# Performance work log

Measured on AMD Instinct MI355X. Metric: run time of the kernel, lower is better.

Reference implementation:

```python
import jax, jax.numpy as jnp
import numpy as np

DIM = 2048
N_HEADS = 32
N_KV_HEADS = 8
HEAD_DIM = DIM // N_HEADS  # 64
GROUP = N_HEADS // N_KV_HEADS  # 4
ROPE_BASE = 10000.0


def setup_inputs() -> dict:
    key = jax.random.key(0)
    k1, k2, k3, k4, k5 = jax.random.split(key, 5)
    b, s = 1, 2048
    scale = 1.0 / np.sqrt(DIM)
    return {
        "x": jax.random.normal(k1, (b, s, DIM), dtype=jnp.float32),
        # weights stored as (in, out); equivalent math to torch Linear (x @ W.T)
        "wq": jax.random.normal(k2, (DIM, N_HEADS * HEAD_DIM), dtype=jnp.float32) * scale,
        "wk": jax.random.normal(k3, (DIM, N_KV_HEADS * HEAD_DIM), dtype=jnp.float32) * scale,
        "wv": jax.random.normal(k4, (DIM, N_KV_HEADS * HEAD_DIM), dtype=jnp.float32) * scale,
        "wo": jax.random.normal(k5, (N_HEADS * HEAD_DIM, DIM), dtype=jnp.float32) * scale,
    }


def _rope_cos_sin(seq_len, dtype):
    inv_freq = 1.0 / (ROPE_BASE ** (jnp.arange(0, HEAD_DIM, 2, dtype=jnp.float32) / HEAD_DIM))
    t = jnp.arange(seq_len, dtype=jnp.float32)
    freqs = jnp.outer(t, inv_freq)              # [s, hd/2]
    emb = jnp.concatenate([freqs, freqs], -1)   # [s, hd]
    return jnp.cos(emb).astype(dtype), jnp.sin(emb).astype(dtype)


def _rotate_half(x):
    x1, x2 = x[..., : HEAD_DIM // 2], x[..., HEAD_DIM // 2 :]
    return jnp.concatenate([-x2, x1], axis=-1)


def reference(x, wq, wk, wv, wo):
    b, s, _ = x.shape
    q = (x @ wq).reshape(b, s, N_HEADS, HEAD_DIM)
    k = (x @ wk).reshape(b, s, N_KV_HEADS, HEAD_DIM)
    v = (x @ wv).reshape(b, s, N_KV_HEADS, HEAD_DIM)

    cos, sin = _rope_cos_sin(s, x.dtype)
    cos = cos[None, :, None, :]  # [1, s, 1, hd] broadcast over batch & heads
    sin = sin[None, :, None, :]
    q = q * cos + _rotate_half(q) * sin
    k = k * cos + _rotate_half(k) * sin

    # GQA: repeat KV heads (repeat_interleave along head dim)
    k = jnp.repeat(k, GROUP, axis=2)  # [b, s, n_heads, hd]
    v = jnp.repeat(v, GROUP, axis=2)

    q = q.transpose(0, 2, 1, 3)  # [b, h, s, d]
    k = k.transpose(0, 2, 1, 3)
    v = v.transpose(0, 2, 1, 3)

    scores = jnp.einsum("bhqd,bhkd->bhqk", q, k) / jnp.sqrt(jnp.asarray(HEAD_DIM, x.dtype))
    attn = jax.nn.softmax(scores, axis=-1)
    out = jnp.einsum("bhqk,bhkd->bhqd", attn, v)
    out = out.transpose(0, 2, 1, 3).reshape(b, s, N_HEADS * HEAD_DIM)
    return out @ wo
```

## Files before the change

kernel.cpp:

```cpp
#include <hip/hip_runtime.h>
#include <hip/hip_bf16.h>

typedef __bf16 bf16x8 __attribute__((ext_vector_type(8)));
typedef __bf16 bf16x4 __attribute__((ext_vector_type(4)));
typedef __bf16 bf16x2 __attribute__((ext_vector_type(2)));
typedef float fx4 __attribute__((ext_vector_type(4)));
typedef float fx16 __attribute__((ext_vector_type(16)));

#define AS1 __attribute__((address_space(1)))
#define AS3 __attribute__((address_space(3)))

__global__ __launch_bounds__(256) void prep(const float4* __restrict__ X, __bf16* __restrict__ Xb,
                                            const float* __restrict__ wq, const float* __restrict__ wk,
                                            const float* __restrict__ wv, const float* __restrict__ wo,
                                            __bf16* __restrict__ WqkvT, __bf16* __restrict__ WoT) {
    const int bx = blockIdx.x;
    if (bx < 4096) {
        const int i = bx * 256 + threadIdx.x;
        const float4 v = X[i];
        bf16x4 o = { (__bf16)v.x, (__bf16)v.y, (__bf16)v.z, (__bf16)v.w };
        *(bf16x4*)(Xb + (size_t)i * 4) = o;
        return;
    }
    constexpr int K = 2048;
    __shared__ float t[64][33];
    const int tt = bx - 4096;
    const float* W; __bf16* Wt; int N, loc;
    if (tt < 2048)      { W = wq; Wt = WqkvT;                       N = 2048; loc = tt; }
    else if (tt < 2560) { W = wk; Wt = WqkvT + (size_t)2048 * 2048; N = 512;  loc = tt - 2048; }
    else if (tt < 3072) { W = wv; Wt = WqkvT + (size_t)2560 * 2048; N = 512;  loc = tt - 2560; }
    else                { W = wo; Wt = WoT;                         N = 2048; loc = tt - 3072; }
    const int k0 = (loc & 31) * 64, n0 = (loc >> 5) * 32;
    const int tx = threadIdx.x & 31, ty = threadIdx.x >> 5;
#pragma unroll
    for (int i = 0; i < 8; ++i)
        t[ty + i * 8][tx] = W[(size_t)(k0 + ty + i * 8) * N + n0 + tx];
    __syncthreads();
#pragma unroll
    for (int i = 0; i < 4; ++i) {
        const int nn = ty + i * 8;
        bf16x2 o = { (__bf16)t[tx * 2][nn], (__bf16)t[tx * 2 + 1][nn] };
        *(bf16x2*)&Wt[(size_t)(n0 + nn) * K + k0 + tx * 2] = o;
    }
}

#define GEMM_SETUP(Aptr, Btptr)                                                              \
    constexpr int K = 2048;                                                                  \
    __shared__ __align__(16) __bf16 sm[4][8192];                                  \
    const int tid = threadIdx.x;                                                             \
    const int wave = tid >> 6, lane = tid & 63;                                              \
    const int quad = lane >> 4, l16 = lane & 15;                                             \
    const int wm = (wave >> 1) * 64, wn = (wave & 1) * 64;                                   \
    fx4 acc[4][4] = {};                                                                      \
    const int r4 = lane >> 2;                                                                \
    const int c8s = ((lane & 3) ^ ((r4 >> 1) & 3)) * 8;                                      \
    const __bf16* csrc[4]; int cdst[4];                                                      \
    _Pragma("unroll")                                                                        \
    for (int it = 0; it < 4; ++it) {                                                         \
        const int idx = wave * 4 + it;                                                       \
        if (idx < 8) { csrc[it] = (Aptr) + (size_t)(m0 + idx * 16 + r4) * K + c8s;           \
                       cdst[it] = idx * 512 + lane * 8; }                                    \
        else         { csrc[it] = (Btptr) + (size_t)(n0 + (idx - 8) * 16 + r4) * K + c8s;    \
                       cdst[it] = 4096 + (idx - 8) * 512 + lane * 8; }                       \
    }                                                                                        \
    const int colr = (quad ^ ((l16 >> 1) & 3)) * 8;                                          \
    const int arow = (wm + l16) * 32 + colr;                                                 \
    const int brow = 4096 + (wn + l16) * 32 + colr;                                          \
    auto compute = [&](const __bf16* cb) {                                                   \
        bf16x8 af[4], bfr[4];                                                                \
        _Pragma("unroll") for (int i = 0; i < 4; ++i) af[i]  = *(const bf16x8*)&cb[arow + i * 512]; \
        _Pragma("unroll") for (int j = 0; j < 4; ++j) bfr[j] = *(const bf16x8*)&cb[brow + j * 512]; \
        __builtin_amdgcn_s_setprio(1);                                                       \
        _Pragma("unroll") for (int i = 0; i < 4; ++i)                                        \
            _Pragma("unroll") for (int j = 0; j < 4; ++j)                                    \
                acc[i][j] = __builtin_amdgcn_mfma_f32_16x16x32_bf16(af[i], bfr[j], acc[i][j], 0, 0, 0); \
        __builtin_amdgcn_s_setprio(0);                                                       \
    };                                                                                       \
    _Pragma("unroll")                                                                        \
    for (int pt = 0; pt < 3; ++pt)                                                           \
        _Pragma("unroll")                                                                    \
        for (int it = 0; it < 4; ++it)                                                       \
            __builtin_amdgcn_global_load_lds((const AS1 void*)(csrc[it] + pt * 32),          \
                                             (AS3 void*)&sm[pt][cdst[it]], 16, 0, 0);        \
    _Pragma("unroll 1")                                                                      \
    for (int tq = 0; tq < 15; ++tq) {                                                        \
        const int t0 = tq * 4;                                                               \
        _Pragma("unroll")                                                                    \
        for (int u = 0; u < 4; ++u) {                                                        \
            asm volatile("s_waitcnt vmcnt(8) lgkmcnt(0)" ::: "memory");                      \
            __builtin_amdgcn_s_barrier();                                                    \
            __builtin_amdgcn_sched_barrier(0);                                               \
            const int tile = t0 + u + 3;                                                     \
            const int kofs = tile * 32;                                                      \
            _Pragma("unroll")                                                                \
            for (int it = 0; it < 4; ++it)                                                   \
                __builtin_amdgcn_global_load_lds((const AS1 void*)(csrc[it] + kofs),         \
                                                 (AS3 void*)&sm[(u + 3) & 3][cdst[it]], 16, 0, 0); \
            compute(sm[u]);                                                                  \
        }                                                                                    \
    }                                                                                        \
    {                            \
        asm volatile("s_waitcnt vmcnt(8) lgkmcnt(0)" ::: "memory");                          \
        __builtin_amdgcn_s_barrier();                                                        \
        __builtin_amdgcn_sched_barrier(0);                                                   \
        _Pragma("unroll")                                                                    \
        for (int it = 0; it < 4; ++it)                                                       \
            __builtin_amdgcn_global_load_lds((const AS1 void*)(csrc[it] + 63 * 32),          \
                                             (AS3 void*)&sm[3][cdst[it]], 16, 0, 0);         \
        compute(sm[0]);                                                                      \
    }                                                                                        \
    asm volatile("s_waitcnt vmcnt(8) lgkmcnt(0)" ::: "memory"); __builtin_amdgcn_s_barrier();\
    __builtin_amdgcn_sched_barrier(0); compute(sm[1]);                                       \
    asm volatile("s_waitcnt vmcnt(4) lgkmcnt(0)" ::: "memory"); __builtin_amdgcn_s_barrier();\
    __builtin_amdgcn_sched_barrier(0); compute(sm[2]);                                       \
    asm volatile("s_waitcnt vmcnt(0) lgkmcnt(0)" ::: "memory"); __builtin_amdgcn_s_barrier();\
    __builtin_amdgcn_sched_barrier(0); compute(sm[3]);

__global__ __launch_bounds__(256, 2) void gemm_qkv(const __bf16* __restrict__ A, const __bf16* __restrict__ Bt,
                                                   __bf16* __restrict__ Qr, __bf16* __restrict__ Kr,
                                                   __bf16* __restrict__ Vt) {
    const int bid = blockIdx.x;
    const int swz = (bid & 7) * 48 + (bid >> 3);
    const int m0 = (swz & 15) * 128, n0 = (swz >> 4) * 128;

    GEMM_SETUP(A, Bt)

    const int col64 = n0 + wn;
    if (col64 < 2560) {
        const bool isQ = col64 < 2048;
        const float scale = isQ ? 0.18033688011112042f : 1.0f;
        __bf16* base = isQ ? (Qr + (size_t)(col64 >> 6) * 2048 * 64)
                           : (Kr + (size_t)((col64 - 2048) >> 6) * 2048 * 64);
#pragma unroll
        for (int jj = 0; jj < 2; ++jj) {
            const int dlo = jj * 16 + l16;
            const float inv = __builtin_amdgcn_exp2f(-(float)dlo * 0.41524101186092029f);
#pragma unroll
            for (int i = 0; i < 4; ++i)
#pragma unroll
                for (int r = 0; r < 4; ++r) {
                    const int s = m0 + wm + i * 16 + quad * 4 + r;
                    float sn, cs;
                    __sincosf((float)s * inv, &sn, &cs);
                    const float lo = acc[i][jj][r], hv = acc[i][jj + 2][r];
                    base[(size_t)s * 64 + dlo]      = (__bf16)((lo * cs - hv * sn) * scale);
                    base[(size_t)s * 64 + dlo + 32] = (__bf16)((hv * cs + lo * sn) * scale);
                }
        }
    } else {
        __bf16* vb = Vt + (size_t)((col64 - 2560) >> 6) * 64 * 2048;
#pragma unroll
        for (int i = 0; i < 4; ++i)
#pragma unroll
            for (int j = 0; j < 4; ++j) {
                const int d = j * 16 + l16;
                const int s0 = m0 + wm + i * 16 + quad * 4;
                bf16x4 p;
#pragma unroll
                for (int r = 0; r < 4; ++r) p[r] = (__bf16)acc[i][j][r];
                *(bf16x4*)&vb[(size_t)d * 2048 + s0] = p;
            }
    }
}

__global__ __launch_bounds__(256, 2) void gemm_out(const __bf16* __restrict__ A, const __bf16* __restrict__ Bt,
                                                   float* __restrict__ C) {
    const int bid = blockIdx.x;
    const int swz = (bid & 7) * 32 + (bid >> 3);
    const int m0 = (swz & 15) * 128, n0 = (swz >> 4) * 128;

    GEMM_SETUP(A, Bt)

#pragma unroll
    for (int i = 0; i < 4; ++i)
#pragma unroll
        for (int j = 0; j < 4; ++j) {
            const int row = m0 + wm + i * 16 + quad * 4;
            const int col = n0 + wn + j * 16 + l16;
#pragma unroll
            for (int r = 0; r < 4; ++r)
                C[(size_t)(row + r) * 2048 + col] = acc[i][j][r];
        }
}

__global__ __launch_bounds__(512, 4) void flash_attn(const __bf16* __restrict__ Qr, const __bf16* __restrict__ Kr,
                                                     const __bf16* __restrict__ Vt, __bf16* __restrict__ O) {
    constexpr int S = 2048;
    __shared__ __align__(16) __bf16 smem[2][4 * 64 * 72];
    const int qt = blockIdx.x, h = blockIdx.y, kvh = h >> 2;
    const int tid = threadIdx.x, wave = tid >> 6, lane = tid & 63;
    const int grp = wave >> 2, w4 = wave & 3;
    const int l32 = lane & 31, hi = lane >> 5;
    const int goff = grp * 2 * 4608;

    const int qrow = qt * 128 + w4 * 32 + l32;
    const __bf16* qptr = Qr + ((size_t)h * S + qrow) * 64;
    bf16x8 qf[4];
#pragma unroll
    for (int kc = 0; kc < 4; ++kc) qf[kc] = *(const bf16x8*)(qptr + kc * 16 + hi * 8);

    const __bf16* Kbase = Kr + (size_t)kvh * S * 64;
    const __bf16* Vbase = Vt + (size_t)kvh * 64 * S;

    const int gtid = tid & 255;
    const int krow = gtid >> 3;
    const int kcol = (gtid & 7) * 8;
    const int vslot = (kcol & 48) | ((kcol & 8) >> 1);

    bf16x8 kreg0 = *(const bf16x8*)(Kbase + (size_t)(grp * 64 + krow) * 64 + kcol);
    bf16x8 kreg1 = *(const bf16x8*)(Kbase + (size_t)(grp * 64 + 32 + krow) * 64 + kcol);
    bf16x8 vreg0 = *(const bf16x8*)(Vbase + (size_t)krow * S + grp * 64 + kcol);
    bf16x8 vreg1 = *(const bf16x8*)(Vbase + (size_t)(32 + krow) * S + grp * 64 + kcol);

    fx16 ov0, ov1;
#pragma unroll
    for (int i = 0; i < 16; ++i) { ov0[i] = 0.f; ov1[i] = 0.f; }
    float l_acc = 0.f;

    {
        __bf16* nK = &smem[0][goff];
        __bf16* nV = nK + 4608;
        *(bf16x8*)&nK[krow * 72 + kcol] = kreg0;
        *(bf16x8*)&nK[(32 + krow) * 72 + kcol] = kreg1;
        bf16x4 v0lo = { vreg0[0], vreg0[1], vreg0[2], vreg0[3] };
        bf16x4 v0hi = { vreg0[4], vreg0[5], vreg0[6], vreg0[7] };
        bf16x4 v1lo = { vreg1[0], vreg1[1], vreg1[2], vreg1[3] };
        bf16x4 v1hi = { vreg1[4], vreg1[5], vreg1[6], vreg1[7] };
        *(bf16x4*)&nV[krow * 72 + vslot]            = v0lo;
        *(bf16x4*)&nV[krow * 72 + vslot + 8]        = v0hi;
        *(bf16x4*)&nV[(32 + krow) * 72 + vslot]     = v1lo;
        *(bf16x4*)&nV[(32 + krow) * 72 + vslot + 8] = v1hi;
        const int kt1 = 2 + grp;
        kreg0 = *(const bf16x8*)(Kbase + (size_t)(kt1 * 64 + krow) * 64 + kcol);
        kreg1 = *(const bf16x8*)(Kbase + (size_t)(kt1 * 64 + 32 + krow) * 64 + kcol);
        vreg0 = *(const bf16x8*)(Vbase + (size_t)krow * S + kt1 * 64 + kcol);
        vreg1 = *(const bf16x8*)(Vbase + (size_t)(32 + krow) * S + kt1 * 64 + kcol);
    }
    asm volatile("s_waitcnt lgkmcnt(0)" ::: "memory");
    __builtin_amdgcn_s_barrier();
    __builtin_amdgcn_sched_barrier(0);

    for (int it = 0; it < 16; ++it) {
        __bf16* lKg = &smem[it & 1][goff];
        __bf16* lVg = lKg + 4608;

        if (it + 1 < 16) {
            __bf16* nK = &smem[(it + 1) & 1][goff];
            __bf16* nV = nK + 4608;
            *(bf16x8*)&nK[krow * 72 + kcol] = kreg0;
            *(bf16x8*)&nK[(32 + krow) * 72 + kcol] = kreg1;
            bf16x4 v0lo = { vreg0[0], vreg0[1], vreg0[2], vreg0[3] };
            bf16x4 v0hi = { vreg0[4], vreg0[5], vreg0[6], vreg0[7] };
            bf16x4 v1lo = { vreg1[0], vreg1[1], vreg1[2], vreg1[3] };
            bf16x4 v1hi = { vreg1[4], vreg1[5], vreg1[6], vreg1[7] };
            *(bf16x4*)&nV[krow * 72 + vslot]            = v0lo;
            *(bf16x4*)&nV[krow * 72 + vslot + 8]        = v0hi;
            *(bf16x4*)&nV[(32 + krow) * 72 + vslot]     = v1lo;
            *(bf16x4*)&nV[(32 + krow) * 72 + vslot + 8] = v1hi;
            const int it2 = (it + 2 < 16) ? it + 2 : 15;
            const int ktn = it2 * 2 + grp;
            kreg0 = *(const bf16x8*)(Kbase + (size_t)(ktn * 64 + krow) * 64 + kcol);
            kreg1 = *(const bf16x8*)(Kbase + (size_t)(ktn * 64 + 32 + krow) * 64 + kcol);
            vreg0 = *(const bf16x8*)(Vbase + (size_t)krow * S + ktn * 64 + kcol);
            vreg1 = *(const bf16x8*)(Vbase + (size_t)(32 + krow) * S + ktn * 64 + kcol);
        }

        fx16 sc0, sc1;
#pragma unroll
        for (int i = 0; i < 16; ++i) { sc0[i] = 0.f; sc1[i] = 0.f; }
        __builtin_amdgcn_s_setprio(1);
#pragma unroll
        for (int kc = 0; kc < 4; ++kc) {
            const bf16x8 a0 = *(const bf16x8*)&lKg[l32 * 72 + kc * 16 + hi * 8];
            const bf16x8 a1 = *(const bf16x8*)&lKg[(32 + l32) * 72 + kc * 16 + hi * 8];
            sc0 = __builtin_amdgcn_mfma_f32_32x32x16_bf16(a0, qf[kc], sc0, 0, 0, 0);
            sc1 = __builtin_amdgcn_mfma_f32_32x32x16_bf16(a1, qf[kc], sc1, 0, 0, 0);
        }
        __builtin_amdgcn_s_setprio(0);

#pragma unroll
        for (int h2 = 0; h2 < 2; ++h2) {
#pragma unroll
            for (int c = 0; c < 2; ++c) {
                bf16x8 pb;
#pragma unroll
                for (int j = 0; j < 8; ++j) {
                    const float sv = h2 ? sc1[c * 8 + j] : sc0[c * 8 + j];
                    const float p = __builtin_amdgcn_exp2f(sv);
                    l_acc += p;
                    pb[j] = (__bf16)p;
                }
                const int kcv = h2 * 2 + c;
                const bf16x8 va0 = *(const bf16x8*)&lVg[l32 * 72 + kcv * 16 + hi * 8];
                const bf16x8 va1 = *(const bf16x8*)&lVg[(32 + l32) * 72 + kcv * 16 + hi * 8];
                __builtin_amdgcn_s_setprio(1);
                ov0 = __builtin_amdgcn_mfma_f32_32x32x16_bf16(va0, pb, ov0, 0, 0, 0);
                ov1 = __builtin_amdgcn_mfma_f32_32x32x16_bf16(va1, pb, ov1, 0, 0, 0);
                __builtin_amdgcn_s_setprio(0);
            }
        }
        asm volatile("s_waitcnt lgkmcnt(0)" ::: "memory");
        __builtin_amdgcn_s_barrier();
        __builtin_amdgcn_sched_barrier(0);
    }

    const float l_pair = l_acc + __shfl_xor(l_acc, 32, 64);

    fx4* lO = (fx4*)&smem[0][0];
    float* lL = (float*)(&smem[0][0] + 16384);
    if (grp == 1) {
#pragma unroll
        for (int ic = 0; ic < 4; ++ic) {
            fx4 c0, c1;
#pragma unroll
            for (int r = 0; r < 4; ++r) { c0[r] = ov0[ic * 4 + r]; c1[r] = ov1[ic * 4 + r]; }
            lO[(ic * 4 + w4) * 64 + lane] = c0;
            lO[((ic + 4) * 4 + w4) * 64 + lane] = c1;
        }
        if (hi == 0) lL[w4 * 32 + l32] = l_pair;
    }
    __syncthreads();
    if (grp == 0) {
#pragma unroll
        for (int ic = 0; ic < 4; ++ic) {
            const fx4 c0 = lO[(ic * 4 + w4) * 64 + lane];
            const fx4 c1 = lO[((ic + 4) * 4 + w4) * 64 + lane];
#pragma unroll
            for (int r = 0; r < 4; ++r) { ov0[ic * 4 + r] += c0[r]; ov1[ic * 4 + r] += c1[r]; }
        }
        const float inv_l = 1.0f / (l_pair + lL[w4 * 32 + l32]);
#pragma unroll
        for (int dt = 0; dt < 2; ++dt)
#pragma unroll
            for (int rg2 = 0; rg2 < 4; ++rg2) {
                bf16x4 o4;
#pragma unroll
                for (int r = 0; r < 4; ++r)
                    o4[r] = (__bf16)((dt ? ov1[rg2 * 4 + r] : ov0[rg2 * 4 + r]) * inv_l);
                const int col = h * 64 + dt * 32 + rg2 * 8 + hi * 4;
                *(bf16x4*)(O + (size_t)qrow * 2048 + col) = o4;
            }
    }
}

extern "C" void kernel_launch(void* const* d_in, const int* in_sizes, int n_in,
                              void* d_out, int out_size, void* d_ws, size_t ws_size,
                              hipStream_t stream) {
    const float* x  = (const float*)d_in[0];
    const float* wq = (const float*)d_in[1];
    const float* wk = (const float*)d_in[2];
    const float* wv = (const float*)d_in[3];
    const float* wo = (const float*)d_in[4];
    float* out = (float*)d_out;
    char* ws = (char*)d_ws;

    __bf16* Xb    = (__bf16*)ws;
    __bf16* WqkvT = (__bf16*)(ws + ((size_t)8 << 20));
    __bf16* WoT   = (__bf16*)(ws + ((size_t)20 << 20));
    __bf16* Qr    = (__bf16*)(ws + ((size_t)28 << 20));
    __bf16* Kr    = (__bf16*)(ws + ((size_t)36 << 20));
    __bf16* Vt    = (__bf16*)(ws + ((size_t)38 << 20));
    __bf16* Ob    = (__bf16*)(ws + ((size_t)40 << 20));

    prep<<<4096 + 5120, 256, 0, stream>>>((const float4*)x, Xb, wq, wk, wv, wo, WqkvT, WoT);
    gemm_qkv<<<384, 256, 0, stream>>>(Xb, WqkvT, Qr, Kr, Vt);
    flash_attn<<<dim3(16, 32), 512, 0, stream>>>(Qr, Kr, Vt, Ob);
    gemm_out<<<256, 256, 0, stream>>>(Ob, WoT, out);
}
```

Measured before the change: 199.8 us.

## Use 3-stage GEMM pipeline at higher occupancy; read V straight from global in attention

The GEMM kernels drop from a 4-buffer to a 3-buffer LDS pipeline with prefetch distance 2. The smaller LDS footprint allows the launch bound to go from 2 to 3 blocks per CU, trading latency hiding for occupancy. In flash attention, V no longer goes through LDS: each lane loads its MFMA operand fragments directly from global memory (two 8-byte loads per fragment), interleaved with the exp/PV quarters. This halves the attention LDS buffers and removes the V shuffle stores, but makes the V reads narrower and more latency-exposed.

```diff
diff --git a/kernel.cpp b/kernel.cpp
--- a/kernel.cpp
+++ b/kernel.cpp
@@ -44,9 +44,14 @@
     }
 }
 
+#define GL(p, d) __builtin_amdgcn_global_load_lds((const AS1 void*)(p), (AS3 void*)(d), 16, 0, 0)
+#define WBAR(N)  asm volatile("s_waitcnt vmcnt(" #N ") lgkmcnt(0)" ::: "memory");             \
+                 __builtin_amdgcn_s_barrier();                                                \
+                 __builtin_amdgcn_sched_barrier(0)
+
 #define GEMM_SETUP(Aptr, Btptr)                                                              \
     constexpr int K = 2048;                                                                  \
-    __shared__ __align__(16) __bf16 sm[4][8192];                                  \
+    __shared__ __align__(16) __bf16 sm[3][8192];                                  \
     const int tid = threadIdx.x;                                                             \
     const int wave = tid >> 6, lane = tid & 63;                                              \
     const int quad = lane >> 4, l16 = lane & 15;                                             \
@@ -77,46 +82,31 @@
         __builtin_amdgcn_s_setprio(0);                                                       \
     };                                                                                       \
     _Pragma("unroll")                                                                        \
-    for (int pt = 0; pt < 3; ++pt)                                                           \
+    for (int pt = 0; pt < 2; ++pt)                                                           \
         _Pragma("unroll")                                                                    \
         for (int it = 0; it < 4; ++it)                                                       \
-            __builtin_amdgcn_global_load_lds((const AS1 void*)(csrc[it] + pt * 32),          \
-                                             (AS3 void*)&sm[pt][cdst[it]], 16, 0, 0);        \
+            GL(csrc[it] + pt * 32, &sm[pt][cdst[it]]);                                       \
     _Pragma("unroll 1")                                                                      \
-    for (int tq = 0; tq < 15; ++tq) {                                                        \
-        const int t0 = tq * 4;                                                               \
+    for (int tq = 0; tq < 20; ++tq) {                                                        \
         _Pragma("unroll")                                                                    \
-        for (int u = 0; u < 4; ++u) {                                                        \
-            asm volatile("s_waitcnt vmcnt(8) lgkmcnt(0)" ::: "memory");                      \
-            __builtin_amdgcn_s_barrier();                                                    \
-            __builtin_amdgcn_sched_barrier(0);                                               \
-            const int tile = t0 + u + 3;                                                     \
-            const int kofs = tile * 32;                                                      \
+        for (int u = 0; u < 3; ++u) {                                                        \
+            const int t = tq * 3 + u;                                                        \
+            WBAR(4);                                                                         \
+            const int kofs = (t + 2) * 32;                                                   \
             _Pragma("unroll")                                                                \
             for (int it = 0; it < 4; ++it)                                                   \
-                __builtin_amdgcn_global_load_lds((const AS1 void*)(csrc[it] + kofs),         \
-                                                 (AS3 void*)&sm[(u + 3) & 3][cdst[it]], 16, 0, 0); \
+                GL(csrc[it] + kofs, &sm[(u + 2) % 3][cdst[it]]);                             \
             compute(sm[u]);                                                                  \
         }                                                                                    \
     }                                                                                        \
-    {                            \
-        asm volatile("s_waitcnt vmcnt(8) lgkmcnt(0)" ::: "memory");                          \
-        __builtin_amdgcn_s_barrier();                                                        \
-        __builtin_amdgcn_sched_barrier(0);                                                   \
-        _Pragma("unroll")                                                                    \
-        for (int it = 0; it < 4; ++it)                                                       \
-            __builtin_amdgcn_global_load_lds((const AS1 void*)(csrc[it] + 63 * 32),          \
-                                             (AS3 void*)&sm[3][cdst[it]], 16, 0, 0);         \
-        compute(sm[0]);                                                                      \
-    }                                                                                        \
-    asm volatile("s_waitcnt vmcnt(8) lgkmcnt(0)" ::: "memory"); __builtin_amdgcn_s_barrier();\
-    __builtin_amdgcn_sched_barrier(0); compute(sm[1]);                                       \
-    asm volatile("s_waitcnt vmcnt(4) lgkmcnt(0)" ::: "memory"); __builtin_amdgcn_s_barrier();\
-    __builtin_amdgcn_sched_barrier(0); compute(sm[2]);                                       \
-    asm volatile("s_waitcnt vmcnt(0) lgkmcnt(0)" ::: "memory"); __builtin_amdgcn_s_barrier();\
-    __builtin_amdgcn_sched_barrier(0); compute(sm[3]);
-
-__global__ __launch_bounds__(256, 2) void gemm_qkv(const __bf16* __restrict__ A, const __bf16* __restrict__ Bt,
+    { WBAR(4); _Pragma("unroll") for (int it = 0; it < 4; ++it)                              \
+          GL(csrc[it] + 62 * 32, &sm[2][cdst[it]]); compute(sm[0]); }              \
+    { WBAR(4); _Pragma("unroll") for (int it = 0; it < 4; ++it)                              \
+          GL(csrc[it] + 63 * 32, &sm[0][cdst[it]]); compute(sm[1]); }              \
+    { WBAR(4); compute(sm[2]); }                                                   \
+    { WBAR(0); compute(sm[0]); }
+
+__global__ __launch_bounds__(256, 3) void gemm_qkv(const __bf16* __restrict__ A, const __bf16* __restrict__ Bt,
                                                    __bf16* __restrict__ Qr, __bf16* __restrict__ Kr,
                                                    __bf16* __restrict__ Vt) {
     const int bid = blockIdx.x;
@@ -163,7 +153,7 @@
     }
 }
 
-__global__ __launch_bounds__(256, 2) void gemm_out(const __bf16* __restrict__ A, const __bf16* __restrict__ Bt,
+__global__ __launch_bounds__(256, 3) void gemm_out(const __bf16* __restrict__ A, const __bf16* __restrict__ Bt,
                                                    float* __restrict__ C) {
     const int bid = blockIdx.x;
     const int swz = (bid & 7) * 32 + (bid >> 3);
@@ -186,12 +176,12 @@
 __global__ __launch_bounds__(512, 4) void flash_attn(const __bf16* __restrict__ Qr, const __bf16* __restrict__ Kr,
                                                      const __bf16* __restrict__ Vt, __bf16* __restrict__ O) {
     constexpr int S = 2048;
-    __shared__ __align__(16) __bf16 smem[2][4 * 64 * 72];
+    __shared__ __align__(16) __bf16 smem[2][2 * 4608];
     const int qt = blockIdx.x, h = blockIdx.y, kvh = h >> 2;
     const int tid = threadIdx.x, wave = tid >> 6, lane = tid & 63;
     const int grp = wave >> 2, w4 = wave & 3;
     const int l32 = lane & 31, hi = lane >> 5;
-    const int goff = grp * 2 * 4608;
+    const int goff = grp * 4608;
 
     const int qrow = qt * 128 + w4 * 32 + l32;
     const __bf16* qptr = Qr + ((size_t)h * S + qrow) * 64;
@@ -201,16 +191,15 @@
 
     const __bf16* Kbase = Kr + (size_t)kvh * S * 64;
     const __bf16* Vbase = Vt + (size_t)kvh * 64 * S;
+    const __bf16* vr0 = Vbase + (size_t)l32 * S + hi * 4;
+    const __bf16* vr1 = Vbase + (size_t)(32 + l32) * S + hi * 4;
 
     const int gtid = tid & 255;
     const int krow = gtid >> 3;
     const int kcol = (gtid & 7) * 8;
-    const int vslot = (kcol & 48) | ((kcol & 8) >> 1);
 
     bf16x8 kreg0 = *(const bf16x8*)(Kbase + (size_t)(grp * 64 + krow) * 64 + kcol);
     bf16x8 kreg1 = *(const bf16x8*)(Kbase + (size_t)(grp * 64 + 32 + krow) * 64 + kcol);
-    bf16x8 vreg0 = *(const bf16x8*)(Vbase + (size_t)krow * S + grp * 64 + kcol);
-    bf16x8 vreg1 = *(const bf16x8*)(Vbase + (size_t)(32 + krow) * S + grp * 64 + kcol);
 
     fx16 ov0, ov1;
 #pragma unroll
@@ -219,51 +208,54 @@
 
     {
         __bf16* nK = &smem[0][goff];
-        __bf16* nV = nK + 4608;
         *(bf16x8*)&nK[krow * 72 + kcol] = kreg0;
         *(bf16x8*)&nK[(32 + krow) * 72 + kcol] = kreg1;
-        bf16x4 v0lo = { vreg0[0], vreg0[1], vreg0[2], vreg0[3] };
-        bf16x4 v0hi = { vreg0[4], vreg0[5], vreg0[6], vreg0[7] };
-        bf16x4 v1lo = { vreg1[0], vreg1[1], vreg1[2], vreg1[3] };
-        bf16x4 v1hi = { vreg1[4], vreg1[5], vreg1[6], vreg1[7] };
-        *(bf16x4*)&nV[krow * 72 + vslot]            = v0lo;
-        *(bf16x4*)&nV[krow * 72 + vslot + 8]        = v0hi;
-        *(bf16x4*)&nV[(32 + krow) * 72 + vslot]     = v1lo;
-        *(bf16x4*)&nV[(32 + krow) * 72 + vslot + 8] = v1hi;
         const int kt1 = 2 + grp;
         kreg0 = *(const bf16x8*)(Kbase + (size_t)(kt1 * 64 + krow) * 64 + kcol);
         kreg1 = *(const bf16x8*)(Kbase + (size_t)(kt1 * 64 + 32 + krow) * 64 + kcol);
-        vreg0 = *(const bf16x8*)(Vbase + (size_t)krow * S + kt1 * 64 + kcol);
-        vreg1 = *(const bf16x8*)(Vbase + (size_t)(32 + krow) * S + kt1 * 64 + kcol);
     }
     asm volatile("s_waitcnt lgkmcnt(0)" ::: "memory");
     __builtin_amdgcn_s_barrier();
     __builtin_amdgcn_sched_barrier(0);
 
+#define VLD8(p) ({ const bf16x4 _a = *(const bf16x4*)(p);                     \
+                   const bf16x4 _b = *(const bf16x4*)((p) + 8);               \
+                   bf16x8 _r = { _a[0],_a[1],_a[2],_a[3], _b[0],_b[1],_b[2],_b[3] }; _r; })
+
+#define QUARTER(SC, C, VA, VB) do {                                           \
+        bf16x8 pb; fx4 p0, p1;                                                \
+        _Pragma("unroll")                                                     \
+        for (int j = 0; j < 4; ++j) {                                         \
+            p0[j] = __builtin_amdgcn_exp2f((SC)[(C) * 8 + j]);                \
+            p1[j] = __builtin_amdgcn_exp2f((SC)[(C) * 8 + 4 + j]);            \
+            pb[j] = (__bf16)p0[j];                                            \
+            pb[4 + j] = (__bf16)p1[j];                                        \
+        }                                                                     \
+        l_acc += ((p0[0] + p0[1]) + (p0[2] + p0[3]))                          \
+               + ((p1[0] + p1[1]) + (p1[2] + p1[3]));                         \
+        __builtin_amdgcn_s_setprio(1);                                        \
+        ov0 = __builtin_amdgcn_mfma_f32_32x32x16_bf16((VA), pb, ov0, 0, 0, 0);\
+        ov1 = __builtin_amdgcn_mfma_f32_32x32x16_bf16((VB), pb, ov1, 0, 0, 0);\
+        __builtin_amdgcn_s_setprio(0);                                        \
+    } while (0)
+
     for (int it = 0; it < 16; ++it) {
-        __bf16* lKg = &smem[it & 1][goff];
-        __bf16* lVg = lKg + 4608;
+        const int kt = it * 2 + grp;
+        const __bf16* lKg = &smem[it & 1][goff];
+        const size_t cb = (size_t)kt * 64;
 
         if (it + 1 < 16) {
             __bf16* nK = &smem[(it + 1) & 1][goff];
-            __bf16* nV = nK + 4608;
             *(bf16x8*)&nK[krow * 72 + kcol] = kreg0;
             *(bf16x8*)&nK[(32 + krow) * 72 + kcol] = kreg1;
-            bf16x4 v0lo = { vreg0[0], vreg0[1], vreg0[2], vreg0[3] };
-            bf16x4 v0hi = { vreg0[4], vreg0[5], vreg0[6], vreg0[7] };
-            bf16x4 v1lo = { vreg1[0], vreg1[1], vreg1[2], vreg1[3] };
-            bf16x4 v1hi = { vreg1[4], vreg1[5], vreg1[6], vreg1[7] };
-            *(bf16x4*)&nV[krow * 72 + vslot]            = v0lo;
-            *(bf16x4*)&nV[krow * 72 + vslot + 8]        = v0hi;
-            *(bf16x4*)&nV[(32 + krow) * 72 + vslot]     = v1lo;
-            *(bf16x4*)&nV[(32 + krow) * 72 + vslot + 8] = v1hi;
             const int it2 = (it + 2 < 16) ? it + 2 : 15;
             const int ktn = it2 * 2 + grp;
             kreg0 = *(const bf16x8*)(Kbase + (size_t)(ktn * 64 + krow) * 64 + kcol);
             kreg1 = *(const bf16x8*)(Kbase + (size_t)(ktn * 64 + 32 + krow) * 64 + kcol);
-            vreg0 = *(const bf16x8*)(Vbase + (size_t)krow * S + ktn * 64 + kcol);
-            vreg1 = *(const bf16x8*)(Vbase + (size_t)(32 + krow) * S + ktn * 64 + kcol);
-        }
+        }
+
+        bf16x8 v00 = VLD8(vr0 + cb);       bf16x8 v01 = VLD8(vr1 + cb);
+        bf16x8 v10 = VLD8(vr0 + cb + 16);  bf16x8 v11 = VLD8(vr1 + cb + 16);
 
         fx16 sc0, sc1;
 #pragma unroll
@@ -278,27 +270,13 @@
         }
         __builtin_amdgcn_s_setprio(0);
 
-#pragma unroll
-        for (int h2 = 0; h2 < 2; ++h2) {
-#pragma unroll
-            for (int c = 0; c < 2; ++c) {
-                bf16x8 pb;
-#pragma unroll
-                for (int j = 0; j < 8; ++j) {
-                    const float sv = h2 ? sc1[c * 8 + j] : sc0[c * 8 + j];
-                    const float p = __builtin_amdgcn_exp2f(sv);
-                    l_acc += p;
-                    pb[j] = (__bf16)p;
-                }
-                const int kcv = h2 * 2 + c;
-                const bf16x8 va0 = *(const bf16x8*)&lVg[l32 * 72 + kcv * 16 + hi * 8];
-                const bf16x8 va1 = *(const bf16x8*)&lVg[(32 + l32) * 72 + kcv * 16 + hi * 8];
-                __builtin_amdgcn_s_setprio(1);
-                ov0 = __builtin_amdgcn_mfma_f32_32x32x16_bf16(va0, pb, ov0, 0, 0, 0);
-                ov1 = __builtin_amdgcn_mfma_f32_32x32x16_bf16(va1, pb, ov1, 0, 0, 0);
-                __builtin_amdgcn_s_setprio(0);
-            }
-        }
+        QUARTER(sc0, 0, v00, v01);
+        bf16x8 v20 = VLD8(vr0 + cb + 32);  bf16x8 v21 = VLD8(vr1 + cb + 32);
+        bf16x8 v30 = VLD8(vr0 + cb + 48);  bf16x8 v31 = VLD8(vr1 + cb + 48);
+        QUARTER(sc0, 1, v10, v11);
+        QUARTER(sc1, 0, v20, v21);
+        QUARTER(sc1, 1, v30, v31);
+
         asm volatile("s_waitcnt lgkmcnt(0)" ::: "memory");
         __builtin_amdgcn_s_barrier();
         __builtin_amdgcn_sched_barrier(0);
@@ -307,7 +285,7 @@
     const float l_pair = l_acc + __shfl_xor(l_acc, 32, 64);
 
     fx4* lO = (fx4*)&smem[0][0];
-    float* lL = (float*)(&smem[0][0] + 16384);
+    float* lL = (float*)((char*)&smem[0][0] + 32768);
     if (grp == 1) {
 #pragma unroll
         for (int ic = 0; ic < 4; ++ic) {
```

Measured after the change: 302.7 us. 1.51x slower.

## Shrink GEMM LDS pipeline to three stages for higher occupancy; tree-sum softmax row

Applied to the files above, without the earlier changes.

The GEMM mainloop goes from a 4-buffer, 3-ahead prefetch to a 3-buffer, 2-ahead prefetch. This cuts shared memory per block from 64KB to 48KB so launch bounds can allow 3 blocks per CU instead of 2. The point is to hide latency with more resident waves rather than deeper prefetch, at the cost of less prefetch distance and tighter register limits. Separately, the attention kernel replaces the serial accumulation of exp values into the row sum with a pairwise tree sum, shortening the dependency chain.

```diff
diff --git a/kernel.cpp b/kernel.cpp
--- a/kernel.cpp
+++ b/kernel.cpp
@@ -44,9 +44,14 @@
     }
 }
 
+#define GL(p, d) __builtin_amdgcn_global_load_lds((const AS1 void*)(p), (AS3 void*)(d), 16, 0, 0)
+#define WBAR(N)  asm volatile("s_waitcnt vmcnt(" #N ") lgkmcnt(0)" ::: "memory");             \
+                 __builtin_amdgcn_s_barrier();                                                \
+                 __builtin_amdgcn_sched_barrier(0)
+
 #define GEMM_SETUP(Aptr, Btptr)                                                              \
     constexpr int K = 2048;                                                                  \
-    __shared__ __align__(16) __bf16 sm[4][8192];                                  \
+    __shared__ __align__(16) __bf16 sm[3][8192];                                  \
     const int tid = threadIdx.x;                                                             \
     const int wave = tid >> 6, lane = tid & 63;                                              \
     const int quad = lane >> 4, l16 = lane & 15;                                             \
@@ -77,46 +82,31 @@
         __builtin_amdgcn_s_setprio(0);                                                       \
     };                                                                                       \
     _Pragma("unroll")                                                                        \
-    for (int pt = 0; pt < 3; ++pt)                                                           \
+    for (int pt = 0; pt < 2; ++pt)                                                           \
         _Pragma("unroll")                                                                    \
         for (int it = 0; it < 4; ++it)                                                       \
-            __builtin_amdgcn_global_load_lds((const AS1 void*)(csrc[it] + pt * 32),          \
-                                             (AS3 void*)&sm[pt][cdst[it]], 16, 0, 0);        \
+            GL(csrc[it] + pt * 32, &sm[pt][cdst[it]]);                                       \
     _Pragma("unroll 1")                                                                      \
-    for (int tq = 0; tq < 15; ++tq) {                                                        \
-        const int t0 = tq * 4;                                                               \
+    for (int tq = 0; tq < 20; ++tq) {                                                        \
         _Pragma("unroll")                                                                    \
-        for (int u = 0; u < 4; ++u) {                                                        \
-            asm volatile("s_waitcnt vmcnt(8) lgkmcnt(0)" ::: "memory");                      \
-            __builtin_amdgcn_s_barrier();                                                    \
-            __builtin_amdgcn_sched_barrier(0);                                               \
-            const int tile = t0 + u + 3;                                                     \
-            const int kofs = tile * 32;                                                      \
+        for (int u = 0; u < 3; ++u) {                                                        \
+            const int t = tq * 3 + u;                                                        \
+            WBAR(4);                                                                         \
+            const int kofs = (t + 2) * 32;                                                   \
             _Pragma("unroll")                                                                \
             for (int it = 0; it < 4; ++it)                                                   \
-                __builtin_amdgcn_global_load_lds((const AS1 void*)(csrc[it] + kofs),         \
-                                                 (AS3 void*)&sm[(u + 3) & 3][cdst[it]], 16, 0, 0); \
+                GL(csrc[it] + kofs, &sm[(u + 2) % 3][cdst[it]]);                             \
             compute(sm[u]);                                                                  \
         }                                                                                    \
     }                                                                                        \
-    {                            \
-        asm volatile("s_waitcnt vmcnt(8) lgkmcnt(0)" ::: "memory");                          \
-        __builtin_amdgcn_s_barrier();                                                        \
-        __builtin_amdgcn_sched_barrier(0);                                                   \
-        _Pragma("unroll")                                                                    \
-        for (int it = 0; it < 4; ++it)                                                       \
-            __builtin_amdgcn_global_load_lds((const AS1 void*)(csrc[it] + 63 * 32),          \
-                                             (AS3 void*)&sm[3][cdst[it]], 16, 0, 0);         \
-        compute(sm[0]);                                                                      \
-    }                                                                                        \
-    asm volatile("s_waitcnt vmcnt(8) lgkmcnt(0)" ::: "memory"); __builtin_amdgcn_s_barrier();\
-    __builtin_amdgcn_sched_barrier(0); compute(sm[1]);                                       \
-    asm volatile("s_waitcnt vmcnt(4) lgkmcnt(0)" ::: "memory"); __builtin_amdgcn_s_barrier();\
-    __builtin_amdgcn_sched_barrier(0); compute(sm[2]);                                       \
-    asm volatile("s_waitcnt vmcnt(0) lgkmcnt(0)" ::: "memory"); __builtin_amdgcn_s_barrier();\
-    __builtin_amdgcn_sched_barrier(0); compute(sm[3]);
-
-__global__ __launch_bounds__(256, 2) void gemm_qkv(const __bf16* __restrict__ A, const __bf16* __restrict__ Bt,
+    { WBAR(4); _Pragma("unroll") for (int it = 0; it < 4; ++it)                              \
+          GL(csrc[it] + 62 * 32, &sm[2][cdst[it]]); compute(sm[0]); }              \
+    { WBAR(4); _Pragma("unroll") for (int it = 0; it < 4; ++it)                              \
+          GL(csrc[it] + 63 * 32, &sm[0][cdst[it]]); compute(sm[1]); }              \
+    { WBAR(4); compute(sm[2]); }                                                   \
+    { WBAR(0); compute(sm[0]); }
+
+__global__ __launch_bounds__(256, 3) void gemm_qkv(const __bf16* __restrict__ A, const __bf16* __restrict__ Bt,
                                                    __bf16* __restrict__ Qr, __bf16* __restrict__ Kr,
                                                    __bf16* __restrict__ Vt) {
     const int bid = blockIdx.x;
@@ -163,7 +153,7 @@
     }
 }
 
-__global__ __launch_bounds__(256, 2) void gemm_out(const __bf16* __restrict__ A, const __bf16* __restrict__ Bt,
+__global__ __launch_bounds__(256, 3) void gemm_out(const __bf16* __restrict__ A, const __bf16* __restrict__ Bt,
                                                    float* __restrict__ C) {
     const int bid = blockIdx.x;
     const int swz = (bid & 7) * 32 + (bid >> 3);
@@ -282,14 +272,15 @@
         for (int h2 = 0; h2 < 2; ++h2) {
 #pragma unroll
             for (int c = 0; c < 2; ++c) {
-                bf16x8 pb;
+                bf16x8 pb; float ps[8];
 #pragma unroll
                 for (int j = 0; j < 8; ++j) {
                     const float sv = h2 ? sc1[c * 8 + j] : sc0[c * 8 + j];
-                    const float p = __builtin_amdgcn_exp2f(sv);
-                    l_acc += p;
-                    pb[j] = (__bf16)p;
+                    ps[j] = __builtin_amdgcn_exp2f(sv);
+                    pb[j] = (__bf16)ps[j];
                 }
+                l_acc += ((ps[0] + ps[1]) + (ps[2] + ps[3]))
+                       + ((ps[4] + ps[5]) + (ps[6] + ps[7]));
                 const int kcv = h2 * 2 + c;
                 const bf16x8 va0 = *(const bf16x8*)&lVg[l32 * 72 + kcv * 16 + hi * 8];
                 const bf16x8 va1 = *(const bf16x8*)&lVg[(32 + l32) * 72 + kcv * 16 + hi * 8];
```

Measured after the change: 200.6 us. Within noise of the previous version (+0.4%).
